# Performance work log

Hardware: AMD Instinct MI355X
Metric: run time of the kernel (lower is better)

Reference implementation:

```python
import jax, jax.numpy as jnp
import numpy as np

HEADS = 8
BUCKETS = 64
TEMP = 0.75
SINKHORN_ITER = 5
EPS = 1e-6


def setup_inputs() -> dict:
    key = jax.random.key(0)
    ks = jax.random.split(key, 6)
    b, t, d = 2, 4096, 1024
    x = jax.random.normal(ks[0], (b, t, d), dtype=jnp.float32)
    gumbel_u = jax.random.uniform(ks[1], (b * HEADS, BUCKETS, BUCKETS), dtype=jnp.float32)
    w_qkv = jax.random.normal(ks[2], (d, 3 * d), dtype=jnp.float32) * (d ** -0.5)
    sort_w = jax.random.normal(ks[3], (1, HEADS, (d // HEADS) * 2, BUCKETS), dtype=jnp.float32)
    w_out = jax.random.normal(ks[4], (d, d), dtype=jnp.float32) * (d ** -0.5)
    b_out = jax.random.normal(ks[5], (d,), dtype=jnp.float32) * 0.01
    return {"x": x, "gumbel_u": gumbel_u, "w_qkv": w_qkv, "sort_w": sort_w,
            "w_out": w_out, "b_out": b_out}


def reference(x, gumbel_u, w_qkv, sort_w, w_out, b_out):
    b, t, d = x.shape
    h, buckets = HEADS, BUCKETS
    d_h = d // h
    bsz = t // buckets
    bh = b * h

    # qkv projection (no bias) and head merge -> (b*h, t, d_h)
    qkv = x @ w_qkv
    q, k, v = jnp.split(qkv, 3, axis=2)
    def merge_heads(u):
        return u.reshape(b, t, h, d_h).transpose(0, 2, 1, 3).reshape(bh, t, d_h)
    q, k, v = merge_heads(q), merge_heads(k), merge_heads(v)

    # bucket -> (bh, buckets, bsz, d_h)
    b_q = q.reshape(bh, buckets, bsz, d_h)
    b_k = k.reshape(bh, buckets, bsz, d_h)
    b_v = v.reshape(bh, buckets, bsz, d_h)

    # SortNet: bucket sums -> leaky_relu(x @ W), W per-head (2*d_h, buckets)
    sx = jnp.concatenate([b_q.sum(axis=2), b_k.sum(axis=2)], axis=-1)  # (bh, buckets, 2*d_h)
    W = jnp.broadcast_to(sort_w, (b, h, 2 * d_h, buckets)).reshape(bh, 2 * d_h, buckets)
    R = jax.nn.leaky_relu(jnp.einsum('bue,bec->buc', sx, W), negative_slope=0.01)

    # gumbel-sinkhorn (log clamped for finiteness; matches torch when R >= 0)
    g = -jnp.log(-jnp.log(gumbel_u + EPS) + EPS)
    r = (jnp.log(jnp.maximum(R + EPS, EPS)) + g) / TEMP
    for _ in range(SINKHORN_ITER):
        r = r - jax.nn.logsumexp(r, axis=2, keepdims=True)
        r = r - jax.nn.logsumexp(r, axis=1, keepdims=True)
    R = jnp.exp(r)

    # zero all but top-1 along last dim
    idx = jnp.argmax(R, axis=2)
    R = jnp.where(jnp.arange(buckets)[None, None, :] == idx[..., None], R, 0.0)

    # soft-permute buckets of k and v, concat with locals -> (bh, buckets, 2*bsz, d_h)
    k_r = jnp.einsum('buv,bvtd->butd', R, b_k)
    v_r = jnp.einsum('buv,bvtd->butd', R, b_v)
    b_k2 = jnp.concatenate([k_r, b_k], axis=2)
    b_v2 = jnp.concatenate([v_r, b_v], axis=2)

    # bucketed attention; NOTE: scale uses full model dim d (as in source)
    dots = jnp.einsum('buie,buje->buij', b_q, b_k2) * (d ** -0.5)
    attn = jax.nn.softmax(dots, axis=-1)
    out = jnp.einsum('buij,buje->buie', attn, b_v2)  # (bh, buckets, bsz, d_h)

    out = out.reshape(b, h, t, d_h).transpose(0, 2, 1, 3).reshape(b, t, d)
    return out @ w_out + b_out
```

## Files before the change

### kernel.cpp

```cpp
#include <hip/hip_runtime.h>
#include <stdint.h>

#define TEMP_ 0.75f
#define EPS_ 1e-6f

typedef __attribute__((ext_vector_type(8))) short bf16x8;
typedef __attribute__((ext_vector_type(4))) float f32x4;

typedef __attribute__((address_space(1))) void gvoid_t;
typedef __attribute__((address_space(3))) void lvoid_t;

__device__ __forceinline__ void async_ld16(const void* g, void* l) {
  __builtin_amdgcn_global_load_lds((gvoid_t*)g, (lvoid_t*)l, 16, 0, 0);
}

__device__ __forceinline__ float b2f(ushort u) {
  return __builtin_bit_cast(float, (uint32_t)u << 16);
}
__device__ __forceinline__ ushort f2b(float f) {
  uint32_t x = __builtin_bit_cast(uint32_t, f);
  x += 0x7fffu + ((x >> 16) & 1u);
  return (ushort)(x >> 16);
}

__global__ __launch_bounds__(256) void prep_x(
    const float* __restrict__ x, ushort* __restrict__ xb, float* __restrict__ xsum2) {
  const int blk = blockIdx.x;
  const int bu = blk >> 1, half = blk & 1;
  const int b = bu >> 6, u = bu & 63;
  const int c = threadIdx.x * 4;
  const float* src = x + ((size_t)(b * 4096 + u * 64 + half * 32)) * 1024 + c;
  ushort* dst = xb + ((size_t)(b * 4096 + u * 64 + half * 32)) * 1024 + c;
  float s0 = 0.f, s1 = 0.f, s2 = 0.f, s3 = 0.f;
  for (int pos = 0; pos < 32; pos++) {
    float4 v = *(const float4*)(src + (size_t)pos * 1024);
    s0 += v.x; s1 += v.y; s2 += v.z; s3 += v.w;
    ushort4 o;
    o.x = f2b(v.x); o.y = f2b(v.y); o.z = f2b(v.z); o.w = f2b(v.w);
    *(ushort4*)(dst + (size_t)pos * 1024) = o;
  }
  float4 sv = {s0, s1, s2, s3};
  *(float4*)&xsum2[(size_t)blk * 1024 + c] = sv;
}

__global__ __launch_bounds__(256) void transpose_f2b(
    const float* __restrict__ src, ushort* __restrict__ dst, int R, int C) {
  __shared__ float tile[32][33];
  int bx = blockIdx.x * 32;
  int by = blockIdx.y * 32;
  int tx = threadIdx.x & 31, ty = threadIdx.x >> 5;
  #pragma unroll
  for (int i = 0; i < 32; i += 8)
    tile[ty + i][tx] = src[(size_t)(by + ty + i) * C + bx + tx];
  __syncthreads();
  #pragma unroll
  for (int i = 0; i < 32; i += 8)
    dst[(size_t)(bx + ty + i) * R + by + tx] = f2b(tile[tx][ty + i]);
}

__global__ __launch_bounds__(256) void sx_gemm_partial(
    const float* __restrict__ xsum2, const float* __restrict__ wqkv,
    float* __restrict__ SXP) {
  __shared__ float xs[128 * 8];
  const int cb = blockIdx.x;
  const int rt = blockIdx.y;
  const int kc = blockIdx.z;
  const int tid = threadIdx.x;
  for (int idx = tid; idx < 1024; idx += 256) {
    int k = idx >> 3, r = idx & 7;
    int bu = rt * 8 + r;
    int kk = kc * 128 + k;
    xs[idx] = xsum2[(size_t)(bu * 2) * 1024 + kk] + xsum2[(size_t)(bu * 2 + 1) * 1024 + kk];
  }
  __syncthreads();
  const int n = cb * 256 + tid;
  float acc[8];
  #pragma unroll
  for (int r = 0; r < 8; r++) acc[r] = 0.f;
  for (int k = 0; k < 128; k++) {
    float w = wqkv[(size_t)(kc * 128 + k) * 3072 + n];
    float4 a0 = *(const float4*)&xs[k * 8];
    float4 a1 = *(const float4*)&xs[k * 8 + 4];
    acc[0] += a0.x * w; acc[1] += a0.y * w; acc[2] += a0.z * w; acc[3] += a0.w * w;
    acc[4] += a1.x * w; acc[5] += a1.y * w; acc[6] += a1.z * w; acc[7] += a1.w * w;
  }
  #pragma unroll
  for (int r = 0; r < 8; r++)
    SXP[(size_t)(kc * 128 + rt * 8 + r) * 2048 + n] = acc[r];
}

__global__ __launch_bounds__(256) void sx_reduce(
    const float* __restrict__ SXP, float* __restrict__ SX) {
  const int bu = blockIdx.y;
  const int n = blockIdx.x * 256 + threadIdx.x;
  float s = 0.f;
  #pragma unroll
  for (int kc = 0; kc < 8; kc++)
    s += SXP[(size_t)(kc * 128 + bu) * 2048 + n];
  const int head = (n >> 7) & 7;
  const int e2 = ((n >> 10) << 7) | (n & 127);
  const int b = bu >> 6, u = bu & 63;
  SX[((size_t)((b * 8 + head) * 256) + e2) * 64 + u] = s;
}

__global__ __launch_bounds__(256) void sortnet_sinkhorn(
    const float* __restrict__ SX, const float* __restrict__ sortw,
    const float* __restrict__ gum, int* __restrict__ idxArr,
    float* __restrict__ wgtArr) {
  __shared__ float sxl[64 * 64];
  __shared__ float wl[64 * 64];
  __shared__ float rr[64 * 65];
  __shared__ float redA[256];
  __shared__ float redB[256];
  __shared__ int redi[256];
  const int bh = blockIdx.x, tid = threadIdx.x, head = bh & 7;
  const int ui = tid & 15, ci = tid >> 4;

  float acc[4][4];
  #pragma unroll
  for (int i = 0; i < 4; i++)
    #pragma unroll
    for (int j = 0; j < 4; j++) acc[i][j] = 0.f;

  const f32x4* SX4 = (const f32x4*)(SX + (size_t)bh * 16384);
  const f32x4* W4 = (const f32x4*)(sortw + (size_t)head * 16384);
  f32x4* sxl4 = (f32x4*)sxl;
  f32x4* wl4 = (f32x4*)wl;

  #pragma unroll 1
  for (int ch = 0; ch < 4; ch++) {
    __syncthreads();
    #pragma unroll 1
    for (int g = tid; g < 1024; g += 256) {
      sxl4[g] = SX4[ch * 1024 + g];
      wl4[g] = W4[ch * 1024 + g];
    }
    __syncthreads();
    #pragma unroll 2
    for (int e = 0; e < 64; e++) {
      f32x4 a = sxl4[e * 16 + ui];
      f32x4 w = wl4[e * 16 + ci];
      #pragma unroll
      for (int i = 0; i < 4; i++)
        #pragma unroll
        for (int j = 0; j < 4; j++) acc[i][j] += a[i] * w[j];
    }
  }

  #pragma unroll
  for (int i = 0; i < 4; i++)
    #pragma unroll
    for (int j = 0; j < 4; j++) {
      int u = ui * 4 + i, c = ci * 4 + j;
      float dot = acc[i][j];
      float r0 = dot > 0.f ? dot : 0.01f * dot;
      float gu = gum[(size_t)bh * 4096 + u * 64 + c];
      float inner = -logf(gu + EPS_) + EPS_;
      float g = -logf(fmaxf(inner, 1e-38f));
      rr[u * 65 + c] = (logf(fmaxf(r0 + EPS_, EPS_)) + g) / TEMP_;
    }
  __syncthreads();

  const int su = tid & 63, sq = tid >> 6;
  #pragma unroll 1
  for (int it = 0; it < 5; it++) {
    {
      float pm = -1e30f;
      #pragma unroll
      for (int j = 0; j < 16; j++) pm = fmaxf(pm, rr[su * 65 + sq * 16 + j]);
      redA[sq * 64 + su] = pm;
      __syncthreads();
      float m = fmaxf(fmaxf(redA[su], redA[64 + su]), fmaxf(redA[128 + su], redA[192 + su]));
      float ps = 0.f;
      #pragma unroll
      for (int j = 0; j < 16; j++) ps += expf(rr[su * 65 + sq * 16 + j] - m);
      redB[sq * 64 + su] = ps;
      __syncthreads();
      float l = m + logf(redB[su] + redB[64 + su] + redB[128 + su] + redB[192 + su]);
      #pragma unroll
      for (int j = 0; j < 16; j++) rr[su * 65 + sq * 16 + j] -= l;
      __syncthreads();
    }
    {
      float pm = -1e30f;
      #pragma unroll
      for (int j = 0; j < 16; j++) pm = fmaxf(pm, rr[(sq * 16 + j) * 65 + su]);
      redA[sq * 64 + su] = pm;
      __syncthreads();
      float m = fmaxf(fmaxf(redA[su], redA[64 + su]), fmaxf(redA[128 + su], redA[192 + su]));
      float ps = 0.f;
      #pragma unroll
      for (int j = 0; j < 16; j++) ps += expf(rr[(sq * 16 + j) * 65 + su] - m);
      redB[sq * 64 + su] = ps;
      __syncthreads();
      float l = m + logf(redB[su] + redB[64 + su] + redB[128 + su] + redB[192 + su]);
      #pragma unroll
      for (int j = 0; j < 16; j++) rr[(sq * 16 + j) * 65 + su] -= l;
      __syncthreads();
    }
  }

  {
    float pv = -1e30f;
    int pi = 0;
    #pragma unroll
    for (int j = 0; j < 16; j++) {
      float v = rr[su * 65 + sq * 16 + j];
      if (v > pv) { pv = v; pi = sq * 16 + j; }
    }
    redA[sq * 64 + su] = pv;
    redi[sq * 64 + su] = pi;
    __syncthreads();
    if (tid < 64) {
      float best = -1e30f;
      int bi = 0;
      #pragma unroll
      for (int q = 0; q < 4; q++) {
        float v = redA[q * 64 + tid];
        if (v > best) { best = v; bi = redi[q * 64 + tid]; }
      }
      idxArr[bh * 64 + tid] = bi;
      wgtArr[bh * 64 + tid] = expf(fminf(best, 80.f));
    }
  }
}

__global__ __launch_bounds__(256, 2) void gemm_bt(
    const ushort* __restrict__ A, const ushort* __restrict__ BT,
    int M, int N, int K, int mode,
    const float* __restrict__ bias, float* __restrict__ Cout,
    ushort* __restrict__ Qb, ushort* __restrict__ Kb, ushort* __restrict__ VT) {
  __shared__ ushort As_lo[128 * 32];
  __shared__ ushort As_hi[128 * 32];
  __shared__ ushort Bs_lo[128 * 32];
  __shared__ ushort Bs_hi[128 * 32];
  const int tid = threadIdx.x;
  const int wave = tid >> 6, lane = tid & 63;
  const int quad = lane >> 4, l16 = lane & 15;
  const int m0 = blockIdx.y * 128, n0 = blockIdx.x * 128;
  const int wm = (wave >> 1) * 64, wn = (wave & 1) * 64;

  f32x4 acc[4][4];
  #pragma unroll
  for (int i = 0; i < 4; i++)
    #pragma unroll
    for (int j = 0; j < 4; j++) acc[i][j] = (f32x4){0.f, 0.f, 0.f, 0.f};

  const int srow = wave * 32 + (lane >> 2);
  const int schunk = (lane & 3) * 8;

  for (int k0 = 0; k0 < K; k0 += 64) {
    __syncthreads();
    {
      const ushort* gA0 = A + (uint64_t)(m0 + srow) * K + k0 + schunk;
      const ushort* gB0 = BT + (uint64_t)(n0 + srow) * K + k0 + schunk;
      const int lofs = (wave * 32) * 32;
      async_ld16(gA0, (ushort*)As_lo + lofs);
      async_ld16(gA0 + (uint64_t)16 * K, (ushort*)As_lo + lofs + 16 * 32);
      async_ld16(gA0 + 32, (ushort*)As_hi + lofs);
      async_ld16(gA0 + (uint64_t)16 * K + 32, (ushort*)As_hi + lofs + 16 * 32);
      async_ld16(gB0, (ushort*)Bs_lo + lofs);
      async_ld16(gB0 + (uint64_t)16 * K, (ushort*)Bs_lo + lofs + 16 * 32);
      async_ld16(gB0 + 32, (ushort*)Bs_hi + lofs);
      async_ld16(gB0 + (uint64_t)16 * K + 32, (ushort*)Bs_hi + lofs + 16 * 32);
    }
    __syncthreads();
    #pragma unroll
    for (int kk = 0; kk < 2; kk++) {
      const ushort* Ab = kk ? As_hi : As_lo;
      const ushort* Bb = kk ? Bs_hi : Bs_lo;
      bf16x8 af[4], bfr[4];
      #pragma unroll
      for (int mt = 0; mt < 4; mt++)
        af[mt] = *(const bf16x8*)&Ab[(wm + mt * 16 + l16) * 32 + quad * 8];
      #pragma unroll
      for (int nt = 0; nt < 4; nt++)
        bfr[nt] = *(const bf16x8*)&Bb[(wn + nt * 16 + l16) * 32 + quad * 8];
      #pragma unroll
      for (int mt = 0; mt < 4; mt++)
        #pragma unroll
        for (int nt = 0; nt < 4; nt++)
          acc[mt][nt] = __builtin_amdgcn_mfma_f32_16x16x32_bf16(af[mt], bfr[nt], acc[mt][nt], 0, 0, 0);
    }
  }

  if (mode == 0) {
    #pragma unroll
    for (int mt = 0; mt < 4; mt++) {
      int row = m0 + wm + mt * 16 + quad * 4;
      #pragma unroll
      for (int nt = 0; nt < 4; nt++) {
        int col = n0 + wn + nt * 16 + l16;
        float bv = bias[col];
        #pragma unroll
        for (int r = 0; r < 4; r++)
          Cout[(uint64_t)(row + r) * N + col] = acc[mt][nt][r] + bv;
      }
    }
  } else {
    int which = blockIdx.x >> 3;
    int head = blockIdx.x & 7;
    #pragma unroll
    for (int mt = 0; mt < 4; mt++) {
      int mrow = m0 + wm + mt * 16 + quad * 4;
      int bidx = mrow >> 12;
      int ttok = mrow & 4095;
      int u = ttok >> 6, pos = ttok & 63;
      int bh = bidx * 8 + head;
      #pragma unroll
      for (int nt = 0; nt < 4; nt++) {
        int e = wn + nt * 16 + l16;
        if (which == 2) {
          ushort4 pk;
          pk.x = f2b(acc[mt][nt][0]);
          pk.y = f2b(acc[mt][nt][1]);
          pk.z = f2b(acc[mt][nt][2]);
          pk.w = f2b(acc[mt][nt][3]);
          *(ushort4*)&VT[((uint64_t)(bh * 64 + u) * 128 + e) * 64 + pos] = pk;
        } else {
          ushort* dst = (which == 0) ? Qb : Kb;
          #pragma unroll
          for (int r = 0; r < 4; r++)
            dst[((uint64_t)(bh * 64 + u) * 64 + pos + r) * 128 + e] = f2b(acc[mt][nt][r]);
        }
      }
    }
  }
}

#define GK 1024

__device__ __forceinline__ void stage32(const ushort* __restrict__ G, int k0,
                                        ushort* lds, int wv, int ln) {
  #pragma unroll
  for (int q = 0; q < 2; ++q) {
    int p = q * 512 + wv * 64 + ln;
    int row = p >> 2;
    int cc = (p & 3) ^ ((row >> 1) & 3);
    async_ld16(G + (size_t)row * GK + k0 + cc * 8,
               lds + (size_t)(q * 512 + wv * 64) * 8);
  }
}

__device__ __forceinline__ bf16x8 ldfrag32(const ushort* buf, int row, int q) {
  int pc = q ^ ((row >> 1) & 3);
  return *(const bf16x8*)&buf[row * 32 + pc * 8];
}

__global__ __launch_bounds__(512, 2) void gemm256_qkv(
    const ushort* __restrict__ A, const ushort* __restrict__ BT,
    ushort* __restrict__ Qb, ushort* __restrict__ Kb, ushort* __restrict__ VT) {
  __shared__ ushort As[4][256 * 32];
  __shared__ ushort Bs[4][256 * 32];
  const int tid = threadIdx.x;
  const int wv = tid >> 6, ln = tid & 63;
  const int quad = ln >> 4, l16 = ln & 15;
  const int wm = (wv >> 2) * 128;
  const int wn = (wv & 3) * 64;
  const int m0 = blockIdx.y * 256, n0 = blockIdx.x * 256;
  const ushort* Ag = A + (size_t)m0 * GK;
  const ushort* Bg = BT + (size_t)n0 * GK;

  f32x4 acc[8][4];
  #pragma unroll
  for (int i = 0; i < 8; i++)
    #pragma unroll
    for (int j = 0; j < 4; j++) acc[i][j] = (f32x4){0.f, 0.f, 0.f, 0.f};

  auto tile = [&](int t) {
    const ushort* Ab = As[t & 3];
    const ushort* Bb = Bs[t & 3];
    bf16x8 a[8], b[4];
    #pragma unroll
    for (int mt = 0; mt < 8; ++mt)
      a[mt] = ldfrag32(Ab, wm + mt * 16 + l16, quad);
    #pragma unroll
    for (int nt = 0; nt < 4; ++nt)
      b[nt] = ldfrag32(Bb, wn + nt * 16 + l16, quad);
    __builtin_amdgcn_s_setprio(1);
    #pragma unroll
    for (int mt = 0; mt < 8; ++mt)
      #pragma unroll
      for (int nt = 0; nt < 4; ++nt)
        acc[mt][nt] = __builtin_amdgcn_mfma_f32_16x16x32_bf16(a[mt], b[nt], acc[mt][nt], 0, 0, 0);
    __builtin_amdgcn_s_setprio(0);
  };

  stage32(Ag, 0, As[0], wv, ln);
  stage32(Bg, 0, Bs[0], wv, ln);
  stage32(Ag, 32, As[1], wv, ln);
  stage32(Bg, 32, Bs[1], wv, ln);
  stage32(Ag, 64, As[2], wv, ln);
  stage32(Bg, 64, Bs[2], wv, ln);

  #pragma unroll 1
  for (int t = 0; t < 30; ++t) {
    asm volatile("s_waitcnt vmcnt(8)\n\ts_barrier" ::: "memory");
    __builtin_amdgcn_sched_barrier(0);
    if (t < 29) {
      int tn = t + 3;
      stage32(Ag, tn * 32, As[tn & 3], wv, ln);
      stage32(Bg, tn * 32, Bs[tn & 3], wv, ln);
    }
    tile(t);
  }
  asm volatile("s_waitcnt vmcnt(4)\n\ts_barrier" ::: "memory");
  __builtin_amdgcn_sched_barrier(0);
  tile(30);
  asm volatile("s_waitcnt vmcnt(0)\n\ts_barrier" ::: "memory");
  __builtin_amdgcn_sched_barrier(0);
  tile(31);

  const int which = n0 >> 10;
  #pragma unroll
  for (int mt = 0; mt < 8; ++mt) {
    int mrow = m0 + wm + mt * 16 + quad * 4;
    int bidx = mrow >> 12;
    int ttok = mrow & 4095;
    int u = ttok >> 6, pos = ttok & 63;
    #pragma unroll
    for (int nt = 0; nt < 4; ++nt) {
      int col = n0 + wn + nt * 16 + l16;
      int head = (col >> 7) & 7;
      int e = col & 127;
      int bh = bidx * 8 + head;
      if (which == 2) {
        ushort4 pk;
        pk.x = f2b(acc[mt][nt][0]);
        pk.y = f2b(acc[mt][nt][1]);
        pk.z = f2b(acc[mt][nt][2]);
        pk.w = f2b(acc[mt][nt][3]);
        *(ushort4*)&VT[((uint64_t)(bh * 64 + u) * 128 + e) * 64 + pos] = pk;
      } else {
        ushort* dst = (which == 0) ? Qb : Kb;
        #pragma unroll
        for (int r = 0; r < 4; ++r)
          dst[((uint64_t)(bh * 64 + u) * 64 + pos + r) * 128 + e] = f2b(acc[mt][nt][r]);
      }
    }
  }
}

#define KSTR 136
__global__ __launch_bounds__(256) void attn_kernel(
    const ushort* __restrict__ Qb, const ushort* __restrict__ Kb,
    const ushort* __restrict__ VT, const int* __restrict__ idxArr,
    const float* __restrict__ wgtArr, ushort* __restrict__ attn_out) {
  __shared__ ushort Qs[64 * KSTR];
  __shared__ ushort Ks[128 * KSTR];
  const int blk = blockIdx.x;
  const int u = blk & 63, bh = blk >> 6;
  const int tid = threadIdx.x, wave = tid >> 6, lane = tid & 63;
  const int quad = lane >> 4, l16 = lane & 15;
  const int vu = idxArr[bh * 64 + u] & 63;
  const float w = wgtArr[bh * 64 + u];

  const ushort* Qsrc = Qb + (uint64_t)(bh * 64 + u) * 8192;
  const ushort* Ksrc0 = Kb + (uint64_t)(bh * 64 + vu) * 8192;
  const ushort* Ksrc1 = Kb + (uint64_t)(bh * 64 + u) * 8192;
  const ushort* Vsrc0 = VT + (uint64_t)(bh * 64 + vu) * 8192;
  const ushort* Vsrc1 = VT + (uint64_t)(bh * 64 + u) * 8192;

  for (int g = tid; g < 64 * 16; g += 256) {
    int eb = g & 15, p = g >> 4;
    *(bf16x8*)&Qs[p * KSTR + eb * 8] = *(const bf16x8*)&Qsrc[p * 128 + eb * 8];
  }
  for (int g = tid; g < 128 * 16; g += 256) {
    int eb = g & 15, j = g >> 4;
    const ushort* s = (j < 64) ? &Ksrc0[j * 128 + eb * 8] : &Ksrc1[(j - 64) * 128 + eb * 8];
    *(bf16x8*)&Ks[j * KSTR + eb * 8] = *(const bf16x8*)s;
  }
  __syncthreads();

  f32x4 S[8];
  #pragma unroll
  for (int nt = 0; nt < 8; nt++) S[nt] = (f32x4){0.f, 0.f, 0.f, 0.f};
  #pragma unroll
  for (int kk = 0; kk < 4; kk++) {
    bf16x8 aq = *(const bf16x8*)&Qs[(wave * 16 + l16) * KSTR + kk * 32 + quad * 8];
    #pragma unroll
    for (int nt = 0; nt < 8; nt++) {
      bf16x8 bk = *(const bf16x8*)&Ks[(nt * 16 + l16) * KSTR + kk * 32 + quad * 8];
      S[nt] = __builtin_amdgcn_mfma_f32_16x16x32_bf16(aq, bk, S[nt], 0, 0, 0);
    }
  }
  __syncthreads();

  for (int g = tid; g < 128 * 16; g += 256) {
    int jb = g & 15, e = g >> 4;
    const ushort* s = (jb < 8) ? &Vsrc0[e * 64 + jb * 8] : &Vsrc1[e * 64 + (jb - 8) * 8];
    *(bf16x8*)&Ks[e * KSTR + jb * 8] = *(const bf16x8*)s;
  }

  const float scale = 0.03125f;
  float rowmax[4] = {-1e30f, -1e30f, -1e30f, -1e30f};
  #pragma unroll
  for (int nt = 0; nt < 8; nt++) {
    float cs = scale * ((nt < 4) ? w : 1.0f);
    #pragma unroll
    for (int r = 0; r < 4; r++) {
      S[nt][r] *= cs;
      rowmax[r] = fmaxf(rowmax[r], S[nt][r]);
    }
  }
  #pragma unroll
  for (int off = 1; off < 16; off <<= 1)
    #pragma unroll
    for (int r = 0; r < 4; r++)
      rowmax[r] = fmaxf(rowmax[r], __shfl_xor(rowmax[r], off, 64));
  float rowsum[4] = {0.f, 0.f, 0.f, 0.f};
  #pragma unroll
  for (int nt = 0; nt < 8; nt++)
    #pragma unroll
    for (int r = 0; r < 4; r++) {
      float p = expf(S[nt][r] - rowmax[r]);
      S[nt][r] = p;
      rowsum[r] += p;
    }
  #pragma unroll
  for (int off = 1; off < 16; off <<= 1)
    #pragma unroll
    for (int r = 0; r < 4; r++)
      rowsum[r] += __shfl_xor(rowsum[r], off, 64);
  float rinv[4];
  #pragma unroll
  for (int r = 0; r < 4; r++) rinv[r] = 1.0f / rowsum[r];

  #pragma unroll
  for (int nt = 0; nt < 8; nt++)
    #pragma unroll
    for (int r = 0; r < 4; r++) {
      float pv = S[nt][r] * rinv[r] * ((nt < 4) ? w : 1.0f);
      Qs[(wave * 16 + quad * 4 + r) * KSTR + nt * 16 + l16] = f2b(pv);
    }
  __syncthreads();

  f32x4 O[8];
  #pragma unroll
  for (int nt = 0; nt < 8; nt++) O[nt] = (f32x4){0.f, 0.f, 0.f, 0.f};
  #pragma unroll
  for (int kk = 0; kk < 4; kk++) {
    bf16x8 ap = *(const bf16x8*)&Qs[(wave * 16 + l16) * KSTR + kk * 32 + quad * 8];
    #pragma unroll
    for (int nt = 0; nt < 8; nt++) {
      bf16x8 bv = *(const bf16x8*)&Ks[(nt * 16 + l16) * KSTR + kk * 32 + quad * 8];
      O[nt] = __builtin_amdgcn_mfma_f32_16x16x32_bf16(ap, bv, O[nt], 0, 0, 0);
    }
  }

  const int bidx = bh >> 3, head = bh & 7;
  uint64_t rowbase =
      (uint64_t)(bidx * 4096 + u * 64 + wave * 16 + quad * 4) * 1024 + head * 128;
  #pragma unroll
  for (int nt = 0; nt < 8; nt++)
    #pragma unroll
    for (int r = 0; r < 4; r++)
      attn_out[rowbase + (uint64_t)r * 1024 + nt * 16 + l16] = f2b(O[nt][r]);
}

extern "C" void kernel_launch(void* const* d_in, const int* in_sizes, int n_in,
                              void* d_out, int out_size, void* d_ws, size_t ws_size,
                              hipStream_t stream) {
  (void)in_sizes; (void)n_in; (void)out_size; (void)ws_size;
  const float* x = (const float*)d_in[0];
  const float* gum = (const float*)d_in[1];
  const float* wqkv = (const float*)d_in[2];
  const float* sortw = (const float*)d_in[3];
  const float* wout = (const float*)d_in[4];
  const float* bout = (const float*)d_in[5];
  float* out = (float*)d_out;

  char* ws = (char*)d_ws;
  size_t off = 0;
  auto alloc = [&](size_t bytes) {
    char* p = ws + off;
    off += (bytes + 255) & ~(size_t)255;
    return p;
  };
  ushort* xb = (ushort*)alloc((size_t)8192 * 1024 * 2);
  float* xsum2 = (float*)alloc((size_t)256 * 1024 * 4);
  ushort* wqkvT = (ushort*)alloc((size_t)3072 * 1024 * 2);
  ushort* woutT = (ushort*)alloc((size_t)1024 * 1024 * 2);
  float* SX = (float*)alloc((size_t)16 * 256 * 64 * 4);
  ushort* Qb = (ushort*)alloc((size_t)16 * 64 * 64 * 128 * 2);
  ushort* Kb = (ushort*)alloc((size_t)16 * 64 * 64 * 128 * 2);
  ushort* VT = (ushort*)alloc((size_t)16 * 64 * 128 * 64 * 2);
  int* idxArr = (int*)alloc((size_t)16 * 64 * 4);
  float* wgtArr = (float*)alloc((size_t)16 * 64 * 4);
  ushort* attn = xb;
  float* SXP = (float*)Qb;

  prep_x<<<256, 256, 0, stream>>>(x, xb, xsum2);
  transpose_f2b<<<dim3(3072 / 32, 1024 / 32), 256, 0, stream>>>(wqkv, wqkvT, 1024, 3072);
  transpose_f2b<<<dim3(1024 / 32, 1024 / 32), 256, 0, stream>>>(wout, woutT, 1024, 1024);
  sx_gemm_partial<<<dim3(8, 16, 8), 256, 0, stream>>>(xsum2, wqkv, SXP);
  sx_reduce<<<dim3(8, 128), 256, 0, stream>>>(SXP, SX);
  sortnet_sinkhorn<<<16, 256, 0, stream>>>(SX, sortw, gum, idxArr, wgtArr);
  gemm256_qkv<<<dim3(3072 / 256, 8192 / 256), 512, 0, stream>>>(xb, wqkvT, Qb, Kb, VT);
  attn_kernel<<<16 * 64, 256, 0, stream>>>(Qb, Kb, VT, idxArr, wgtArr, attn);
  gemm_bt<<<dim3(1024 / 128, 8192 / 128), 256, 0, stream>>>(
      attn, woutT, 8192, 1024, 1024, 0, bout, out, nullptr, nullptr, nullptr);
}
```

Before: 290.1 us.

## Retile QKV GEMM to 256x192 blocks with split-phase LDS reads and staging

The QKV projection GEMM moves from 256x256 tiles to 256x192 tiles. The grid grows from 384 to 512 blocks, which divides evenly over the 256 CUs. Each k-step is split into two halves, each reading fragments with inline ds_read_b128 and then issuing the A or B async stage for a future tile. The per-wave wait counts differ because only six waves load B. The Q/K/V destination is now chosen per column because a tile can straddle a 1024 boundary. The changes aim to fix wave quantization and overlap LDS reads with MFMA. The costs are more barriers per k-step, lower arithmetic intensity, and launch bounds dropped to one block per CU.

```diff
diff --git a/kernel.cpp b/kernel.cpp
--- a/kernel.cpp
+++ b/kernel.cpp
@@ -21,6 +21,16 @@
   uint32_t x = __builtin_bit_cast(uint32_t, f);
   x += 0x7fffu + ((x >> 16) & 1u);
   return (ushort)(x >> 16);
+}
+
+__device__ __forceinline__ uint32_t lds_u32(const void* p) {
+  return (uint32_t)(uintptr_t)(lvoid_t*)p;
+}
+
+__device__ __forceinline__ bf16x8 dsr(uint32_t addr) {
+  bf16x8 d;
+  asm volatile("ds_read_b128 %0, %1" : "=v"(d) : "v"(addr));
+  return d;
 }
 
 __global__ __launch_bounds__(256) void prep_x(
@@ -330,88 +340,136 @@
 
 #define GK 1024
 
-__device__ __forceinline__ void stage32(const ushort* __restrict__ G, int k0,
-                                        ushort* lds, int wv, int ln) {
-  #pragma unroll
-  for (int q = 0; q < 2; ++q) {
-    int p = q * 512 + wv * 64 + ln;
-    int row = p >> 2;
-    int cc = (p & 3) ^ ((row >> 1) & 3);
-    async_ld16(G + (size_t)row * GK + k0 + cc * 8,
-               lds + (size_t)(q * 512 + wv * 64) * 8);
-  }
-}
-
-__device__ __forceinline__ bf16x8 ldfrag32(const ushort* buf, int row, int q) {
-  int pc = q ^ ((row >> 1) & 3);
-  return *(const bf16x8*)&buf[row * 32 + pc * 8];
-}
-
-__global__ __launch_bounds__(512, 2) void gemm256_qkv(
+__global__ __launch_bounds__(512, 1) void gemm_qkv192(
     const ushort* __restrict__ A, const ushort* __restrict__ BT,
     ushort* __restrict__ Qb, ushort* __restrict__ Kb, ushort* __restrict__ VT) {
   __shared__ ushort As[4][256 * 32];
-  __shared__ ushort Bs[4][256 * 32];
+  __shared__ ushort Bs[4][192 * 32];
   const int tid = threadIdx.x;
   const int wv = tid >> 6, ln = tid & 63;
   const int quad = ln >> 4, l16 = ln & 15;
   const int wm = (wv >> 2) * 128;
-  const int wn = (wv & 3) * 64;
-  const int m0 = blockIdx.y * 256, n0 = blockIdx.x * 256;
+  const int wn = (wv & 3) * 48;
+  const int m0 = blockIdx.y * 256, n0 = blockIdx.x * 192;
   const ushort* Ag = A + (size_t)m0 * GK;
   const ushort* Bg = BT + (size_t)n0 * GK;
 
-  f32x4 acc[8][4];
+  auto stageA = [&](int tt) {
+    const int k0 = tt * 32, buf = tt & 3;
+    #pragma unroll
+    for (int q = 0; q < 2; ++q) {
+      int p = q * 512 + wv * 64 + ln;
+      int row = p >> 2;
+      int cc = (p & 3) ^ ((row >> 1) & 3);
+      async_ld16(Ag + (size_t)row * GK + k0 + cc * 8,
+                 (ushort*)&As[buf][(q * 512 + wv * 64) * 8]);
+    }
+  };
+  auto stageB = [&](int tt) {
+    if (wv >= 6) return;
+    const int k0 = tt * 32, buf = tt & 3;
+    #pragma unroll
+    for (int q = 0; q < 2; ++q) {
+      int p = wv * 128 + q * 64 + ln;
+      int row = p >> 2;
+      int cc = (p & 3) ^ ((row >> 1) & 3);
+      async_ld16(Bg + (size_t)row * GK + k0 + cc * 8,
+                 (ushort*)&Bs[buf][(wv * 128 + q * 64) * 8]);
+    }
+  };
+
+  const uint32_t asB = lds_u32(&As[0][0]);
+  const uint32_t bsB = lds_u32(&Bs[0][0]);
+  uint32_t aoff[8], boff[3];
+  #pragma unroll
+  for (int mt = 0; mt < 8; ++mt) {
+    int row = wm + mt * 16 + l16;
+    int pc = quad ^ ((row >> 1) & 3);
+    aoff[mt] = (uint32_t)(row * 64 + pc * 16);
+  }
+  #pragma unroll
+  for (int nt = 0; nt < 3; ++nt) {
+    int row = wn + nt * 16 + l16;
+    int pc = quad ^ ((row >> 1) & 3);
+    boff[nt] = (uint32_t)(row * 64 + pc * 16);
+  }
+
+  f32x4 acc[8][3];
   #pragma unroll
   for (int i = 0; i < 8; i++)
     #pragma unroll
-    for (int j = 0; j < 4; j++) acc[i][j] = (f32x4){0.f, 0.f, 0.f, 0.f};
-
-  auto tile = [&](int t) {
-    const ushort* Ab = As[t & 3];
-    const ushort* Bb = Bs[t & 3];
-    bf16x8 a[8], b[4];
-    #pragma unroll
-    for (int mt = 0; mt < 8; ++mt)
-      a[mt] = ldfrag32(Ab, wm + mt * 16 + l16, quad);
-    #pragma unroll
-    for (int nt = 0; nt < 4; ++nt)
-      b[nt] = ldfrag32(Bb, wn + nt * 16 + l16, quad);
+    for (int j = 0; j < 3; j++) acc[i][j] = (f32x4){0.f, 0.f, 0.f, 0.f};
+
+  stageA(0); stageB(0);
+  stageA(1); stageB(1);
+  stageA(2); stageB(2);
+
+  #pragma unroll 1
+  for (int t = 0; t < 32; ++t) {
+    if (t < 30) {
+      if (wv < 6) asm volatile("s_waitcnt vmcnt(8)" ::: "memory");
+      else        asm volatile("s_waitcnt vmcnt(4)" ::: "memory");
+    } else if (t == 30) {
+      if (wv < 6) asm volatile("s_waitcnt vmcnt(4)" ::: "memory");
+      else        asm volatile("s_waitcnt vmcnt(2)" ::: "memory");
+    } else {
+      asm volatile("s_waitcnt vmcnt(0)" ::: "memory");
+    }
+    __builtin_amdgcn_s_barrier();
+
+    const uint32_t ab = asB + (uint32_t)(t & 3) * 16384u;
+    const uint32_t bb = bsB + (uint32_t)(t & 3) * 12288u;
+
+    bf16x8 a0 = dsr(ab + aoff[0]);
+    bf16x8 a1 = dsr(ab + aoff[1]);
+    bf16x8 a2 = dsr(ab + aoff[2]);
+    bf16x8 a3 = dsr(ab + aoff[3]);
+    bf16x8 b0 = dsr(bb + boff[0]);
+    bf16x8 b1 = dsr(bb + boff[1]);
+    bf16x8 b2 = dsr(bb + boff[2]);
+    if (t < 29) stageA(t + 3);
+    __builtin_amdgcn_s_barrier();
+    asm volatile("s_waitcnt lgkmcnt(0)" ::: "memory");
+    __builtin_amdgcn_sched_barrier(0);
     __builtin_amdgcn_s_setprio(1);
-    #pragma unroll
-    for (int mt = 0; mt < 8; ++mt)
-      #pragma unroll
-      for (int nt = 0; nt < 4; ++nt)
-        acc[mt][nt] = __builtin_amdgcn_mfma_f32_16x16x32_bf16(a[mt], b[nt], acc[mt][nt], 0, 0, 0);
+    acc[0][0] = __builtin_amdgcn_mfma_f32_16x16x32_bf16(a0, b0, acc[0][0], 0, 0, 0);
+    acc[0][1] = __builtin_amdgcn_mfma_f32_16x16x32_bf16(a0, b1, acc[0][1], 0, 0, 0);
+    acc[0][2] = __builtin_amdgcn_mfma_f32_16x16x32_bf16(a0, b2, acc[0][2], 0, 0, 0);
+    acc[1][0] = __builtin_amdgcn_mfma_f32_16x16x32_bf16(a1, b0, acc[1][0], 0, 0, 0);
+    acc[1][1] = __builtin_amdgcn_mfma_f32_16x16x32_bf16(a1, b1, acc[1][1], 0, 0, 0);
+    acc[1][2] = __builtin_amdgcn_mfma_f32_16x16x32_bf16(a1, b2, acc[1][2], 0, 0, 0);
+    acc[2][0] = __builtin_amdgcn_mfma_f32_16x16x32_bf16(a2, b0, acc[2][0], 0, 0, 0);
+    acc[2][1] = __builtin_amdgcn_mfma_f32_16x16x32_bf16(a2, b1, acc[2][1], 0, 0, 0);
+    acc[2][2] = __builtin_amdgcn_mfma_f32_16x16x32_bf16(a2, b2, acc[2][2], 0, 0, 0);
+    acc[3][0] = __builtin_amdgcn_mfma_f32_16x16x32_bf16(a3, b0, acc[3][0], 0, 0, 0);
+    acc[3][1] = __builtin_amdgcn_mfma_f32_16x16x32_bf16(a3, b1, acc[3][1], 0, 0, 0);
+    acc[3][2] = __builtin_amdgcn_mfma_f32_16x16x32_bf16(a3, b2, acc[3][2], 0, 0, 0);
     __builtin_amdgcn_s_setprio(0);
-  };
-
-  stage32(Ag, 0, As[0], wv, ln);
-  stage32(Bg, 0, Bs[0], wv, ln);
-  stage32(Ag, 32, As[1], wv, ln);
-  stage32(Bg, 32, Bs[1], wv, ln);
-  stage32(Ag, 64, As[2], wv, ln);
-  stage32(Bg, 64, Bs[2], wv, ln);
-
-  #pragma unroll 1
-  for (int t = 0; t < 30; ++t) {
-    asm volatile("s_waitcnt vmcnt(8)\n\ts_barrier" ::: "memory");
+
+    bf16x8 a4 = dsr(ab + aoff[4]);
+    bf16x8 a5 = dsr(ab + aoff[5]);
+    bf16x8 a6 = dsr(ab + aoff[6]);
+    bf16x8 a7 = dsr(ab + aoff[7]);
+    if (t < 29) stageB(t + 3);
+    __builtin_amdgcn_s_barrier();
+    asm volatile("s_waitcnt lgkmcnt(0)" ::: "memory");
     __builtin_amdgcn_sched_barrier(0);
-    if (t < 29) {
-      int tn = t + 3;
-      stage32(Ag, tn * 32, As[tn & 3], wv, ln);
-      stage32(Bg, tn * 32, Bs[tn & 3], wv, ln);
-    }
-    tile(t);
-  }
-  asm volatile("s_waitcnt vmcnt(4)\n\ts_barrier" ::: "memory");
-  __builtin_amdgcn_sched_barrier(0);
-  tile(30);
-  asm volatile("s_waitcnt vmcnt(0)\n\ts_barrier" ::: "memory");
-  __builtin_amdgcn_sched_barrier(0);
-  tile(31);
-
-  const int which = n0 >> 10;
+    __builtin_amdgcn_s_setprio(1);
+    acc[4][0] = __builtin_amdgcn_mfma_f32_16x16x32_bf16(a4, b0, acc[4][0], 0, 0, 0);
+    acc[4][1] = __builtin_amdgcn_mfma_f32_16x16x32_bf16(a4, b1, acc[4][1], 0, 0, 0);
+    acc[4][2] = __builtin_amdgcn_mfma_f32_16x16x32_bf16(a4, b2, acc[4][2], 0, 0, 0);
+    acc[5][0] = __builtin_amdgcn_mfma_f32_16x16x32_bf16(a5, b0, acc[5][0], 0, 0, 0);
+    acc[5][1] = __builtin_amdgcn_mfma_f32_16x16x32_bf16(a5, b1, acc[5][1], 0, 0, 0);
+    acc[5][2] = __builtin_amdgcn_mfma_f32_16x16x32_bf16(a5, b2, acc[5][2], 0, 0, 0);
+    acc[6][0] = __builtin_amdgcn_mfma_f32_16x16x32_bf16(a6, b0, acc[6][0], 0, 0, 0);
+    acc[6][1] = __builtin_amdgcn_mfma_f32_16x16x32_bf16(a6, b1, acc[6][1], 0, 0, 0);
+    acc[6][2] = __builtin_amdgcn_mfma_f32_16x16x32_bf16(a6, b2, acc[6][2], 0, 0, 0);
+    acc[7][0] = __builtin_amdgcn_mfma_f32_16x16x32_bf16(a7, b0, acc[7][0], 0, 0, 0);
+    acc[7][1] = __builtin_amdgcn_mfma_f32_16x16x32_bf16(a7, b1, acc[7][1], 0, 0, 0);
+    acc[7][2] = __builtin_amdgcn_mfma_f32_16x16x32_bf16(a7, b2, acc[7][2], 0, 0, 0);
+    __builtin_amdgcn_s_setprio(0);
+  }
+
   #pragma unroll
   for (int mt = 0; mt < 8; ++mt) {
     int mrow = m0 + wm + mt * 16 + quad * 4;
@@ -419,8 +477,9 @@
     int ttok = mrow & 4095;
     int u = ttok >> 6, pos = ttok & 63;
     #pragma unroll
-    for (int nt = 0; nt < 4; ++nt) {
+    for (int nt = 0; nt < 3; ++nt) {
       int col = n0 + wn + nt * 16 + l16;
+      int which = col >> 10;
       int head = (col >> 7) & 7;
       int e = col & 127;
       int bh = bidx * 8 + head;
@@ -596,7 +655,7 @@
   sx_gemm_partial<<<dim3(8, 16, 8), 256, 0, stream>>>(xsum2, wqkv, SXP);
   sx_reduce<<<dim3(8, 128), 256, 0, stream>>>(SXP, SX);
   sortnet_sinkhorn<<<16, 256, 0, stream>>>(SX, sortw, gum, idxArr, wgtArr);
-  gemm256_qkv<<<dim3(3072 / 256, 8192 / 256), 512, 0, stream>>>(xb, wqkvT, Qb, Kb, VT);
+  gemm_qkv192<<<dim3(3072 / 192, 8192 / 256), 512, 0, stream>>>(xb, wqkvT, Qb, Kb, VT);
   attn_kernel<<<16 * 64, 256, 0, stream>>>(Qb, Kb, VT, idxArr, wgtArr, attn);
   gemm_bt<<<dim3(1024 / 128, 8192 / 128), 256, 0, stream>>>(
       attn, woutT, 8192, 1024, 1024, 0, bout, out, nullptr, nullptr, nullptr);
```

After: 270.4 us. 1.07x faster.
